# Kernel tuning notes

Measured on AMD Instinct MI355X. Metric: run time of the kernel, lower is better.

The kernel has to match this reference:

```python
import jax, jax.numpy as jnp
import numpy as np

N_NODES = 40000
N_EDGES = 640000


def _sage_conv(x, src, dst, W_nb, b, W_self, n_nodes):
    # message = x[src] gathered per edge; mean-aggregate at dst (PyG SAGEConv, aggr='mean')
    msgs = x[src]  # [E, d]
    agg = jax.ops.segment_sum(msgs, dst, num_segments=n_nodes)  # [N, d]
    deg = jax.ops.segment_sum(jnp.ones((src.shape[0],), dtype=x.dtype), dst, num_segments=n_nodes)
    mean = agg / jnp.maximum(deg, 1.0)[:, None]
    # lin_l(aggregated) with bias + lin_r(self) without bias
    return mean @ W_nb + b + x @ W_self


def setup_inputs() -> dict:
    key = jax.random.key(0)
    ks = jax.random.split(key, 8)
    in_dim, h1, h2, out_dim = 128, 128, 64, 40
    s = lambda k, shp, d: jax.random.normal(k, shp, dtype=jnp.float32) / np.sqrt(d)
    return {
        "x": jax.random.normal(ks[0], (N_NODES, in_dim), dtype=jnp.float32),
        "edge_index": jax.random.randint(ks[1], (2, N_EDGES), 0, N_NODES, dtype=jnp.int64) if jax.config.jax_enable_x64 else jax.random.randint(ks[1], (2, N_EDGES), 0, N_NODES).astype(jnp.int32),
        "W1_nb": s(ks[2], (in_dim, h1), in_dim),
        "b1": jnp.zeros((h1,), dtype=jnp.float32),
        "W1_self": s(ks[3], (in_dim, h1), in_dim),
        "W2_nb": s(ks[4], (h1, h2), h1),
        "b2": jnp.zeros((h2,), dtype=jnp.float32),
        "W2_self": s(ks[5], (h1, h2), h1),
        "Wfc": s(ks[6], (h2, out_dim), h2),
        "bfc": jnp.zeros((out_dim,), dtype=jnp.float32),
    }


def reference(x, edge_index, W1_nb, b1, W1_self, W2_nb, b2, W2_self, Wfc, bfc):
    src, dst = edge_index[0], edge_index[1]
    h = jax.nn.relu(_sage_conv(x, src, dst, W1_nb, b1, W1_self, N_NODES))
    h = jax.nn.relu(_sage_conv(h, src, dst, W2_nb, b2, W2_self, N_NODES))
    embedding = h
    logits = h @ Wfc + bfc
    return (embedding, logits)
```

## Files before the change

kernel.cpp:

```cpp
#include <hip/hip_runtime.h>
#include <hip/hip_bf16.h>


#define N_NODES 40000
#define N_EDGES 640000
#define D_IN    128
#define D_H1    128
#define D_H2    64
#define D_OUT   40

#define SCAN_BLK 1024
#define N_SCAN_BLKS ((N_NODES + SCAN_BLK - 1) / SCAN_BLK)

typedef __attribute__((ext_vector_type(8))) short short8v;
typedef __attribute__((ext_vector_type(4))) float float4v;

__device__ __forceinline__ unsigned short f2bf(float f) {
    unsigned u = __float_as_uint(f);
    unsigned r = u + 0x7FFFu + ((u >> 16) & 1u);
    return (unsigned short)(r >> 16);
}
__device__ __forceinline__ float bf2f(unsigned short b) {
    return __uint_as_float(((unsigned)b) << 16);
}


__global__ void hist_k(const int* __restrict__ dst, int* __restrict__ deg) {
    int e = blockIdx.x * blockDim.x + threadIdx.x;
    if (e < N_EDGES) atomicAdd(&deg[dst[e]], 1);
}

__global__ __launch_bounds__(SCAN_BLK) void scan1_k(const int* __restrict__ deg,
                                                    int* __restrict__ blocksum) {
    __shared__ int wsum[SCAN_BLK / 64];
    int t = threadIdx.x;
    int i = blockIdx.x * SCAN_BLK + t;
    int v = (i < N_NODES) ? deg[i] : 0;
    #pragma unroll
    for (int s = 32; s > 0; s >>= 1) v += __shfl_down(v, s);
    if ((t & 63) == 0) wsum[t >> 6] = v;
    __syncthreads();
    if (t < SCAN_BLK / 64) {
        int x = wsum[t];
        #pragma unroll
        for (int s = SCAN_BLK / 128; s > 0; s >>= 1) x += __shfl_down(x, s);
        if (t == 0) blocksum[blockIdx.x] = x;
    }
}

__global__ void scan2_k(const int* __restrict__ blocksum, int* __restrict__ blockbase,
                        int* __restrict__ offsets) {
    if (threadIdx.x == 0 && blockIdx.x == 0) {
        int acc = 0;
        for (int b = 0; b < N_SCAN_BLKS; b++) { blockbase[b] = acc; acc += blocksum[b]; }
        offsets[N_NODES] = acc;
    }
}

__global__ __launch_bounds__(SCAN_BLK) void scan3_k(const int* __restrict__ deg,
                                                    const int* __restrict__ blockbase,
                                                    int* __restrict__ offsets,
                                                    int* __restrict__ cursor) {
    __shared__ int sm[SCAN_BLK];
    int t = threadIdx.x;
    int i = blockIdx.x * SCAN_BLK + t;
    int v = (i < N_NODES) ? deg[i] : 0;
    sm[t] = v;
    __syncthreads();
    for (int s = 1; s < SCAN_BLK; s <<= 1) {
        int u = (t >= s) ? sm[t - s] : 0;
        __syncthreads();
        sm[t] += u;
        __syncthreads();
    }
    if (i < N_NODES) {
        int excl = blockbase[blockIdx.x] + sm[t] - v;
        offsets[i] = excl;
        cursor[i] = excl;
    }
}

__global__ void place_k(const int* __restrict__ src, const int* __restrict__ dst,
                        int* __restrict__ cursor, int* __restrict__ src_sorted) {
    int e = blockIdx.x * blockDim.x + threadIdx.x;
    if (e < N_EDGES) {
        int p = atomicAdd(&cursor[dst[e]], 1);
        src_sorted[p] = src[e];
    }
}


__global__ __launch_bounds__(256) void agg_k(const float* __restrict__ feat,
                                             const int* __restrict__ offsets,
                                             const int* __restrict__ srcs,
                                             float* __restrict__ mean_out) {
    int t = threadIdx.x;
    int g = t >> 5;
    int q = t & 31;
    int node = blockIdx.x * 8 + g;
    int beg = offsets[node];
    int end = offsets[node + 1];
    float ax = 0.f, ay = 0.f, az = 0.f, aw = 0.f;
    int i = beg;
    for (; i + 4 <= end; i += 4) {
        int s0 = srcs[i], s1 = srcs[i + 1], s2 = srcs[i + 2], s3 = srcs[i + 3];
        float4 v0 = ((const float4*)(feat + (size_t)s0 * 128))[q];
        float4 v1 = ((const float4*)(feat + (size_t)s1 * 128))[q];
        float4 v2 = ((const float4*)(feat + (size_t)s2 * 128))[q];
        float4 v3 = ((const float4*)(feat + (size_t)s3 * 128))[q];
        ax += v0.x + v1.x + v2.x + v3.x;
        ay += v0.y + v1.y + v2.y + v3.y;
        az += v0.z + v1.z + v2.z + v3.z;
        aw += v0.w + v1.w + v2.w + v3.w;
    }
    for (; i < end; ++i) {
        float4 v = ((const float4*)(feat + (size_t)srcs[i] * 128))[q];
        ax += v.x; ay += v.y; az += v.z; aw += v.w;
    }
    int cnt = end - beg;
    float inv = 1.0f / (float)(cnt > 1 ? cnt : 1);
    float4 r; r.x = ax * inv; r.y = ay * inv; r.z = az * inv; r.w = aw * inv;
    ((float4*)(mean_out + (size_t)node * 128))[q] = r;
}


__global__ void wsplit_k(const float* __restrict__ W, int K, int N,
                         short* __restrict__ Wt_hi, short* __restrict__ Wt_lo) {
    int tid = blockIdx.x * blockDim.x + threadIdx.x;
    if (tid >= K * N) return;
    int k = tid / N, n = tid - k * N;
    float w = W[tid];
    unsigned short h = f2bf(w);
    unsigned short lo = f2bf(w - bf2f(h));
    Wt_hi[n * K + k] = (short)h;
    Wt_lo[n * K + k] = (short)lo;
}


template <int NOUT>
__global__ __launch_bounds__(256) void sage_mfma_k(
    const float* __restrict__ A1, const float* __restrict__ A2,
    const short* __restrict__ W1h, const short* __restrict__ W1l,
    const short* __restrict__ W2h, const short* __restrict__ W2l,
    const float* __restrict__ bias, float* __restrict__ out) {
    __shared__ short wh_s[64 * 128];
    __shared__ short wl_s[64 * 128];

    const int t = threadIdx.x;
    const int w = t >> 6;
    const int l = t & 63;
    const int ln16 = l & 15;
    const int kgrp = l >> 4;
    const int arow = blockIdx.x * 32 + (w & 1) * 16 + ln16;
    const int colbase = blockIdx.y * 64;
    const int cw = (w >> 1) * 32;

    float4v acc[2];
    #pragma unroll
    for (int ct = 0; ct < 2; ct++) {
        float bv = bias[colbase + cw + ct * 16 + ln16];
        acc[ct] = (float4v){bv, bv, bv, bv};
    }

    for (int phase = 0; phase < 2; ++phase) {
        const float* __restrict__ A  = phase ? A2 : A1;
        const short* __restrict__ Wh = phase ? W2h : W1h;
        const short* __restrict__ Wl = phase ? W2l : W1l;

        __syncthreads();

        float4 a0[4], a1[4];
        const float* ap = A + (size_t)arow * 128 + kgrp * 8;
        #pragma unroll
        for (int kc = 0; kc < 4; kc++) {
            a0[kc] = *(const float4*)(ap + kc * 32);
            a1[kc] = *(const float4*)(ap + kc * 32 + 4);
        }

        #pragma unroll
        for (int it = 0; it < 4; it++) {
            int fid = t + it * 256;
            int r = fid >> 4, c = fid & 15;
            int gofs = (colbase + r) * 128 + c * 8;
            int byte = (r * 256 + c * 16) ^ ((r & 7) << 4);
            *(int4*)((char*)wh_s + byte) = *(const int4*)(Wh + gofs);
            *(int4*)((char*)wl_s + byte) = *(const int4*)(Wl + gofs);
        }

        short8v ah[4], al[4];
        #pragma unroll
        for (int kc = 0; kc < 4; kc++) {
            #pragma unroll
            for (int j = 0; j < 4; j++) {
                float f0 = (&a0[kc].x)[j];
                float f1 = (&a1[kc].x)[j];
                unsigned short h0 = f2bf(f0), h1 = f2bf(f1);
                ah[kc][j]     = (short)h0;
                ah[kc][j + 4] = (short)h1;
                al[kc][j]     = (short)f2bf(f0 - bf2f(h0));
                al[kc][j + 4] = (short)f2bf(f1 - bf2f(h1));
            }
        }

        __syncthreads();

        #pragma unroll
        for (int kc = 0; kc < 4; kc++) {
            #pragma unroll
            for (int ct = 0; ct < 2; ct++) {
                int col = cw + ct * 16 + ln16;
                int byte = (col * 256 + kc * 64 + kgrp * 16) ^ ((col & 7) << 4);
                short8v bh = *(const short8v*)((const char*)wh_s + byte);
                short8v bl = *(const short8v*)((const char*)wl_s + byte);
                acc[ct] = __builtin_amdgcn_mfma_f32_16x16x32_bf16(ah[kc], bh, acc[ct], 0, 0, 0);
                acc[ct] = __builtin_amdgcn_mfma_f32_16x16x32_bf16(ah[kc], bl, acc[ct], 0, 0, 0);
                acc[ct] = __builtin_amdgcn_mfma_f32_16x16x32_bf16(al[kc], bh, acc[ct], 0, 0, 0);
            }
        }
    }

    #pragma unroll
    for (int ct = 0; ct < 2; ct++) {
        #pragma unroll
        for (int r = 0; r < 4; r++) {
            int row = blockIdx.x * 32 + (w & 1) * 16 + kgrp * 4 + r;
            int col = colbase + cw + ct * 16 + ln16;
            out[(size_t)row * NOUT + col] = fmaxf(acc[ct][r], 0.f);
        }
    }
}


__global__ void fc_k(const float* __restrict__ h2, const float* __restrict__ W,
                     const float* __restrict__ b, float* __restrict__ out) {
    int idx = blockIdx.x * blockDim.x + threadIdx.x;
    if (idx >= N_NODES * D_OUT) return;
    int node = idx / D_OUT;
    int c = idx - node * D_OUT;
    float acc = b[c];
    const float4* h4 = (const float4*)(h2 + (size_t)node * D_H2);
    #pragma unroll
    for (int k4 = 0; k4 < D_H2 / 4; k4++) {
        float4 h = h4[k4];
        acc += h.x * W[(k4 * 4 + 0) * D_OUT + c];
        acc += h.y * W[(k4 * 4 + 1) * D_OUT + c];
        acc += h.z * W[(k4 * 4 + 2) * D_OUT + c];
        acc += h.w * W[(k4 * 4 + 3) * D_OUT + c];
    }
    out[idx] = acc;
}


extern "C" void kernel_launch(void* const* d_in, const int* in_sizes, int n_in,
                              void* d_out, int out_size, void* d_ws, size_t ws_size,
                              hipStream_t stream) {
    const float* x       = (const float*)d_in[0];
    const int*   ei      = (const int*)d_in[1];
    const float* W1_nb   = (const float*)d_in[2];
    const float* b1      = (const float*)d_in[3];
    const float* W1_self = (const float*)d_in[4];
    const float* W2_nb   = (const float*)d_in[5];
    const float* b2      = (const float*)d_in[6];
    const float* W2_self = (const float*)d_in[7];
    const float* Wfc     = (const float*)d_in[8];
    const float* bfc     = (const float*)d_in[9];

    const int* src = ei;
    const int* dst = ei + N_EDGES;

    char* w = (char*)d_ws;
    int* deg        = (int*)w;
    int* offsets    = deg + N_NODES;
    int* cursor     = offsets + (N_NODES + 1);
    int* blocksum   = cursor + N_NODES;
    int* blockbase  = blocksum + N_SCAN_BLKS;
    int* src_sorted = blockbase + N_SCAN_BLKS;
    size_t int_elems = (size_t)N_NODES * 3 + 1 + 2 * N_SCAN_BLKS + N_EDGES;
    size_t int_bytes = (int_elems * 4 + 15) & ~(size_t)15;
    float* mean = (float*)(w + int_bytes);
    float* h1   = mean + (size_t)N_NODES * 128;
    short* w1nb_h   = (short*)(h1 + (size_t)N_NODES * 128);
    short* w1nb_l   = w1nb_h + 128 * 128;
    short* w1self_h = w1nb_l + 128 * 128;
    short* w1self_l = w1self_h + 128 * 128;
    short* w2nb_h   = w1self_l + 128 * 128;
    short* w2nb_l   = w2nb_h + 128 * 64;
    short* w2self_h = w2nb_l + 128 * 64;
    short* w2self_l = w2self_h + 128 * 64;

    float* emb    = (float*)d_out;
    float* logits = emb + (size_t)N_NODES * D_H2;

    wsplit_k<<<(128 * 128 + 255) / 256, 256, 0, stream>>>(W1_nb,   128, 128, w1nb_h,   w1nb_l);
    wsplit_k<<<(128 * 128 + 255) / 256, 256, 0, stream>>>(W1_self, 128, 128, w1self_h, w1self_l);
    wsplit_k<<<(128 * 64  + 255) / 256, 256, 0, stream>>>(W2_nb,   128, 64,  w2nb_h,   w2nb_l);
    wsplit_k<<<(128 * 64  + 255) / 256, 256, 0, stream>>>(W2_self, 128, 64,  w2self_h, w2self_l);

    hipMemsetAsync(deg, 0, N_NODES * sizeof(int), stream);
    hist_k<<<(N_EDGES + 255) / 256, 256, 0, stream>>>(dst, deg);
    scan1_k<<<N_SCAN_BLKS, SCAN_BLK, 0, stream>>>(deg, blocksum);
    scan2_k<<<1, 64, 0, stream>>>(blocksum, blockbase, offsets);
    scan3_k<<<N_SCAN_BLKS, SCAN_BLK, 0, stream>>>(deg, blockbase, offsets, cursor);
    place_k<<<(N_EDGES + 255) / 256, 256, 0, stream>>>(src, dst, cursor, src_sorted);

    agg_k<<<N_NODES / 8, 256, 0, stream>>>(x, offsets, src_sorted, mean);
    sage_mfma_k<128><<<dim3(N_NODES / 32, 2), 256, 0, stream>>>(mean, x, w1nb_h, w1nb_l,
                                                                w1self_h, w1self_l, b1, h1);

    agg_k<<<N_NODES / 8, 256, 0, stream>>>(h1, offsets, src_sorted, mean);
    sage_mfma_k<64><<<dim3(N_NODES / 32, 1), 256, 0, stream>>>(mean, h1, w2nb_h, w2nb_l,
                                                               w2self_h, w2self_l, b2, emb);

    fc_k<<<(N_NODES * D_OUT + 255) / 256, 256, 0, stream>>>(emb, Wfc, bfc, logits);
}
```

Measured before the change: 322.8 us.

## Transform before aggregating in layer 2 and fuse final FC with activation

```diff
diff --git a/kernel.cpp b/kernel.cpp
--- a/kernel.cpp
+++ b/kernel.cpp
@@ -48,22 +48,21 @@
     }
 }
 
-__global__ void scan2_k(const int* __restrict__ blocksum, int* __restrict__ blockbase,
-                        int* __restrict__ offsets) {
-    if (threadIdx.x == 0 && blockIdx.x == 0) {
-        int acc = 0;
-        for (int b = 0; b < N_SCAN_BLKS; b++) { blockbase[b] = acc; acc += blocksum[b]; }
-        offsets[N_NODES] = acc;
-    }
-}
-
 __global__ __launch_bounds__(SCAN_BLK) void scan3_k(const int* __restrict__ deg,
-                                                    const int* __restrict__ blockbase,
+                                                    const int* __restrict__ blocksum,
                                                     int* __restrict__ offsets,
                                                     int* __restrict__ cursor) {
     __shared__ int sm[SCAN_BLK];
+    __shared__ int base_s;
     int t = threadIdx.x;
     int i = blockIdx.x * SCAN_BLK + t;
+    if (t == 0) {
+        int b = 0;
+        for (int j = 0; j < (int)blockIdx.x; j++) b += blocksum[j];
+        base_s = b;
+        if (blockIdx.x == N_SCAN_BLKS - 1)
+            offsets[N_NODES] = b + blocksum[blockIdx.x];
+    }
     int v = (i < N_NODES) ? deg[i] : 0;
     sm[t] = v;
     __syncthreads();
@@ -74,7 +73,7 @@
         __syncthreads();
     }
     if (i < N_NODES) {
-        int excl = blockbase[blockIdx.x] + sm[t] - v;
+        int excl = base_s + sm[t] - v;
         offsets[i] = excl;
         cursor[i] = excl;
     }
@@ -90,50 +89,68 @@
 }
 
 
+template <int D, int STRIDE>
 __global__ __launch_bounds__(256) void agg_k(const float* __restrict__ feat,
                                              const int* __restrict__ offsets,
                                              const int* __restrict__ srcs,
                                              float* __restrict__ mean_out) {
+    constexpr int LPN = D / 4;
+    constexpr int NPB = 256 / LPN;
     int t = threadIdx.x;
-    int g = t >> 5;
-    int q = t & 31;
-    int node = blockIdx.x * 8 + g;
+    int g = t / LPN;
+    int q = t % LPN;
+    int node = blockIdx.x * NPB + g;
     int beg = offsets[node];
     int end = offsets[node + 1];
-    float ax = 0.f, ay = 0.f, az = 0.f, aw = 0.f;
+    float4 accA = {0.f, 0.f, 0.f, 0.f}, accB = {0.f, 0.f, 0.f, 0.f};
     int i = beg;
-    for (; i + 4 <= end; i += 4) {
-        int s0 = srcs[i], s1 = srcs[i + 1], s2 = srcs[i + 2], s3 = srcs[i + 3];
-        float4 v0 = ((const float4*)(feat + (size_t)s0 * 128))[q];
-        float4 v1 = ((const float4*)(feat + (size_t)s1 * 128))[q];
-        float4 v2 = ((const float4*)(feat + (size_t)s2 * 128))[q];
-        float4 v3 = ((const float4*)(feat + (size_t)s3 * 128))[q];
-        ax += v0.x + v1.x + v2.x + v3.x;
-        ay += v0.y + v1.y + v2.y + v3.y;
-        az += v0.z + v1.z + v2.z + v3.z;
-        aw += v0.w + v1.w + v2.w + v3.w;
+    for (; i + 8 <= end; i += 8) {
+        float4 v[8];
+        #pragma unroll
+        for (int j = 0; j < 8; j++) {
+            int s = srcs[i + j];
+            v[j] = *(const float4*)(feat + (size_t)s * STRIDE + q * 4);
+        }
+        #pragma unroll
+        for (int j = 0; j < 4; j++) {
+            accA.x += v[j].x; accA.y += v[j].y; accA.z += v[j].z; accA.w += v[j].w;
+            accB.x += v[j+4].x; accB.y += v[j+4].y; accB.z += v[j+4].z; accB.w += v[j+4].w;
+        }
     }
     for (; i < end; ++i) {
-        float4 v = ((const float4*)(feat + (size_t)srcs[i] * 128))[q];
-        ax += v.x; ay += v.y; az += v.z; aw += v.w;
+        float4 v = *(const float4*)(feat + (size_t)srcs[i] * STRIDE + q * 4);
+        accA.x += v.x; accA.y += v.y; accA.z += v.z; accA.w += v.w;
     }
     int cnt = end - beg;
     float inv = 1.0f / (float)(cnt > 1 ? cnt : 1);
-    float4 r; r.x = ax * inv; r.y = ay * inv; r.z = az * inv; r.w = aw * inv;
-    ((float4*)(mean_out + (size_t)node * 128))[q] = r;
-}
-
-
-__global__ void wsplit_k(const float* __restrict__ W, int K, int N,
-                         short* __restrict__ Wt_hi, short* __restrict__ Wt_lo) {
-    int tid = blockIdx.x * blockDim.x + threadIdx.x;
-    if (tid >= K * N) return;
+    float4 r;
+    r.x = (accA.x + accB.x) * inv; r.y = (accA.y + accB.y) * inv;
+    r.z = (accA.z + accB.z) * inv; r.w = (accA.w + accB.w) * inv;
+    *(float4*)(mean_out + (size_t)node * D + q * 4) = r;
+}
+
+
+__device__ __forceinline__ void wsplit_one(const float* W, int K, int N, int tid,
+                                           short* Wt_hi, short* Wt_lo) {
     int k = tid / N, n = tid - k * N;
     float w = W[tid];
     unsigned short h = f2bf(w);
     unsigned short lo = f2bf(w - bf2f(h));
     Wt_hi[n * K + k] = (short)h;
     Wt_lo[n * K + k] = (short)lo;
+}
+
+__global__ void wsplit_all_k(const float* __restrict__ W1nb, const float* __restrict__ W1sf,
+                             const float* __restrict__ W2nb, const float* __restrict__ W2sf,
+                             short* __restrict__ o1nbh, short* __restrict__ o1nbl,
+                             short* __restrict__ o1sfh, short* __restrict__ o1sfl,
+                             short* __restrict__ o2nbh, short* __restrict__ o2nbl,
+                             short* __restrict__ o2sfh, short* __restrict__ o2sfl) {
+    int tid = blockIdx.x * blockDim.x + threadIdx.x;
+    if (tid < 16384)      wsplit_one(W1nb, 128, 128, tid,          o1nbh, o1nbl);
+    else if (tid < 32768) wsplit_one(W1sf, 128, 128, tid - 16384,  o1sfh, o1sfl);
+    else if (tid < 40960) wsplit_one(W2nb, 128, 64,  tid - 32768,  o2nbh, o2nbl);
+    else if (tid < 49152) wsplit_one(W2sf, 128, 64,  tid - 40960,  o2sfh, o2sfl);
 }
 
 
@@ -231,23 +248,125 @@
 }
 
 
-__global__ void fc_k(const float* __restrict__ h2, const float* __restrict__ W,
-                     const float* __restrict__ b, float* __restrict__ out) {
-    int idx = blockIdx.x * blockDim.x + threadIdx.x;
-    if (idx >= N_NODES * D_OUT) return;
-    int node = idx / D_OUT;
-    int c = idx - node * D_OUT;
-    float acc = b[c];
-    const float4* h4 = (const float4*)(h2 + (size_t)node * D_H2);
-    #pragma unroll
-    for (int k4 = 0; k4 < D_H2 / 4; k4++) {
-        float4 h = h4[k4];
-        acc += h.x * W[(k4 * 4 + 0) * D_OUT + c];
-        acc += h.y * W[(k4 * 4 + 1) * D_OUT + c];
-        acc += h.z * W[(k4 * 4 + 2) * D_OUT + c];
-        acc += h.w * W[(k4 * 4 + 3) * D_OUT + c];
-    }
-    out[idx] = acc;
+__global__ __launch_bounds__(256) void gemm2_k(
+    const float* __restrict__ A,
+    const short* __restrict__ Wnbh, const short* __restrict__ Wnbl,
+    const short* __restrict__ Wsfh, const short* __restrict__ Wsfl,
+    const float* __restrict__ b2, float* __restrict__ zs2) {
+    __shared__ short wh_s[64 * 128];
+    __shared__ short wl_s[64 * 128];
+
+    const int t = threadIdx.x;
+    const int w = t >> 6;
+    const int l = t & 63;
+    const int ln16 = l & 15;
+    const int kgrp = l >> 4;
+    const int arow = blockIdx.x * 32 + (w & 1) * 16 + ln16;
+    const int ysel = blockIdx.y;
+    const int cw = (w >> 1) * 32;
+
+    const short* __restrict__ Wh = ysel ? Wsfh : Wnbh;
+    const short* __restrict__ Wl = ysel ? Wsfl : Wnbl;
+
+    float4v acc[2];
+    #pragma unroll
+    for (int ct = 0; ct < 2; ct++) {
+        float bv = ysel ? b2[cw + ct * 16 + ln16] : 0.f;
+        acc[ct] = (float4v){bv, bv, bv, bv};
+    }
+
+    float4 a0[4], a1[4];
+    const float* ap = A + (size_t)arow * 128 + kgrp * 8;
+    #pragma unroll
+    for (int kc = 0; kc < 4; kc++) {
+        a0[kc] = *(const float4*)(ap + kc * 32);
+        a1[kc] = *(const float4*)(ap + kc * 32 + 4);
+    }
+
+    #pragma unroll
+    for (int it = 0; it < 4; it++) {
+        int fid = t + it * 256;
+        int r = fid >> 4, c = fid & 15;
+        int gofs = r * 128 + c * 8;
+        int byte = (r * 256 + c * 16) ^ ((r & 7) << 4);
+        *(int4*)((char*)wh_s + byte) = *(const int4*)(Wh + gofs);
+        *(int4*)((char*)wl_s + byte) = *(const int4*)(Wl + gofs);
+    }
+
+    short8v ah[4], al[4];
+    #pragma unroll
+    for (int kc = 0; kc < 4; kc++) {
+        #pragma unroll
+        for (int j = 0; j < 4; j++) {
+            float f0 = (&a0[kc].x)[j];
+            float f1 = (&a1[kc].x)[j];
+            unsigned short h0 = f2bf(f0), h1 = f2bf(f1);
+            ah[kc][j]     = (short)h0;
+            ah[kc][j + 4] = (short)h1;
+            al[kc][j]     = (short)f2bf(f0 - bf2f(h0));
+            al[kc][j + 4] = (short)f2bf(f1 - bf2f(h1));
+        }
+    }
+
+    __syncthreads();
+
+    #pragma unroll
+    for (int kc = 0; kc < 4; kc++) {
+        #pragma unroll
+        for (int ct = 0; ct < 2; ct++) {
+            int col = cw + ct * 16 + ln16;
+            int byte = (col * 256 + kc * 64 + kgrp * 16) ^ ((col & 7) << 4);
+            short8v bh = *(const short8v*)((const char*)wh_s + byte);
+            short8v bl = *(const short8v*)((const char*)wl_s + byte);
+            acc[ct] = __builtin_amdgcn_mfma_f32_16x16x32_bf16(ah[kc], bh, acc[ct], 0, 0, 0);
+            acc[ct] = __builtin_amdgcn_mfma_f32_16x16x32_bf16(ah[kc], bl, acc[ct], 0, 0, 0);
+            acc[ct] = __builtin_amdgcn_mfma_f32_16x16x32_bf16(al[kc], bh, acc[ct], 0, 0, 0);
+        }
+    }
+
+    #pragma unroll
+    for (int ct = 0; ct < 2; ct++) {
+        #pragma unroll
+        for (int r = 0; r < 4; r++) {
+            int row = blockIdx.x * 32 + (w & 1) * 16 + kgrp * 4 + r;
+            int col = ysel * 64 + cw + ct * 16 + ln16;
+            zs2[(size_t)row * 128 + col] = acc[ct][r];
+        }
+    }
+}
+
+
+__global__ __launch_bounds__(256) void final_k(const float* __restrict__ mean2,
+                                               const float* __restrict__ zs2,
+                                               const float* __restrict__ Wfc,
+                                               const float* __restrict__ bfc,
+                                               float* __restrict__ emb,
+                                               float* __restrict__ logits) {
+    __shared__ float es[16][68];
+    int t = threadIdx.x;
+    int g = t >> 4;
+    int q = t & 15;
+    int node = blockIdx.x * 16 + g;
+    float4 m = *(const float4*)(mean2 + (size_t)node * 64 + q * 4);
+    float4 s = *(const float4*)(zs2 + (size_t)node * 128 + 64 + q * 4);
+    float4 e;
+    e.x = fmaxf(m.x + s.x, 0.f);
+    e.y = fmaxf(m.y + s.y, 0.f);
+    e.z = fmaxf(m.z + s.z, 0.f);
+    e.w = fmaxf(m.w + s.w, 0.f);
+    *(float4*)(emb + (size_t)node * 64 + q * 4) = e;
+    *(float4*)&es[g][q * 4] = e;
+    __syncthreads();
+    #pragma unroll
+    for (int j = 0; j < 3; j++) {
+        int c = q + 16 * j;
+        if (c < D_OUT) {
+            float acc = bfc[c];
+            #pragma unroll
+            for (int k = 0; k < 64; k++) acc += es[g][k] * Wfc[k * D_OUT + c];
+            logits[(size_t)node * D_OUT + c] = acc;
+        }
+    }
 }
 
 
@@ -273,13 +392,12 @@
     int* offsets    = deg + N_NODES;
     int* cursor     = offsets + (N_NODES + 1);
     int* blocksum   = cursor + N_NODES;
-    int* blockbase  = blocksum + N_SCAN_BLKS;
-    int* src_sorted = blockbase + N_SCAN_BLKS;
-    size_t int_elems = (size_t)N_NODES * 3 + 1 + 2 * N_SCAN_BLKS + N_EDGES;
+    int* src_sorted = blocksum + N_SCAN_BLKS;
+    size_t int_elems = (size_t)N_NODES * 3 + 1 + N_SCAN_BLKS + N_EDGES;
     size_t int_bytes = (int_elems * 4 + 15) & ~(size_t)15;
-    float* mean = (float*)(w + int_bytes);
-    float* h1   = mean + (size_t)N_NODES * 128;
-    short* w1nb_h   = (short*)(h1 + (size_t)N_NODES * 128);
+    float* bufA = (float*)(w + int_bytes);
+    float* bufB = bufA + (size_t)N_NODES * 128;
+    short* w1nb_h   = (short*)(bufB + (size_t)N_NODES * 128);
     short* w1nb_l   = w1nb_h + 128 * 128;
     short* w1self_h = w1nb_l + 128 * 128;
     short* w1self_l = w1self_h + 128 * 128;
@@ -291,25 +409,24 @@
     float* emb    = (float*)d_out;
     float* logits = emb + (size_t)N_NODES * D_H2;
 
-    wsplit_k<<<(128 * 128 + 255) / 256, 256, 0, stream>>>(W1_nb,   128, 128, w1nb_h,   w1nb_l);
-    wsplit_k<<<(128 * 128 + 255) / 256, 256, 0, stream>>>(W1_self, 128, 128, w1self_h, w1self_l);
-    wsplit_k<<<(128 * 64  + 255) / 256, 256, 0, stream>>>(W2_nb,   128, 64,  w2nb_h,   w2nb_l);
-    wsplit_k<<<(128 * 64  + 255) / 256, 256, 0, stream>>>(W2_self, 128, 64,  w2self_h, w2self_l);
+    wsplit_all_k<<<(49152 + 255) / 256, 256, 0, stream>>>(
+        W1_nb, W1_self, W2_nb, W2_self,
+        w1nb_h, w1nb_l, w1self_h, w1self_l, w2nb_h, w2nb_l, w2self_h, w2self_l);
 
     hipMemsetAsync(deg, 0, N_NODES * sizeof(int), stream);
     hist_k<<<(N_EDGES + 255) / 256, 256, 0, stream>>>(dst, deg);
     scan1_k<<<N_SCAN_BLKS, SCAN_BLK, 0, stream>>>(deg, blocksum);
-    scan2_k<<<1, 64, 0, stream>>>(blocksum, blockbase, offsets);
-    scan3_k<<<N_SCAN_BLKS, SCAN_BLK, 0, stream>>>(deg, blockbase, offsets, cursor);
+    scan3_k<<<N_SCAN_BLKS, SCAN_BLK, 0, stream>>>(deg, blocksum, offsets, cursor);
     place_k<<<(N_EDGES + 255) / 256, 256, 0, stream>>>(src, dst, cursor, src_sorted);
 
-    agg_k<<<N_NODES / 8, 256, 0, stream>>>(x, offsets, src_sorted, mean);
-    sage_mfma_k<128><<<dim3(N_NODES / 32, 2), 256, 0, stream>>>(mean, x, w1nb_h, w1nb_l,
-                                                                w1self_h, w1self_l, b1, h1);
-
-    agg_k<<<N_NODES / 8, 256, 0, stream>>>(h1, offsets, src_sorted, mean);
-    sage_mfma_k<64><<<dim3(N_NODES / 32, 1), 256, 0, stream>>>(mean, h1, w2nb_h, w2nb_l,
-                                                               w2self_h, w2self_l, b2, emb);
-
-    fc_k<<<(N_NODES * D_OUT + 255) / 256, 256, 0, stream>>>(emb, Wfc, bfc, logits);
-}
+    agg_k<128, 128><<<N_NODES / 8, 256, 0, stream>>>(x, offsets, src_sorted, bufA);
+    sage_mfma_k<128><<<dim3(N_NODES / 32, 2), 256, 0, stream>>>(
+        bufA, x, w1nb_h, w1nb_l, w1self_h, w1self_l, b1, bufB);
+
+    gemm2_k<<<dim3(N_NODES / 32, 2), 256, 0, stream>>>(
+        bufB, w2nb_h, w2nb_l, w2self_h, w2self_l, b2, bufA);
+
+    agg_k<64, 128><<<N_NODES / 16, 256, 0, stream>>>(bufA, offsets, src_sorted, bufB);
+
+    final_k<<<N_NODES / 16, 256, 0, stream>>>(bufB, bufA, Wfc, bfc, emb, logits);
+}
```

Measured after the change: 294.0 us. 1.1x faster.
